# Kernel optimization log

Measured on AMD Instinct MI355X. Metric: run time of the kernel, lower is better.

Reference implementation:

```python
import jax, jax.numpy as jnp
import numpy as np

D_MODEL = 1024
NUM_HEADS = 16
MAX_LEN = 2048
D_HEAD = D_MODEL // NUM_HEADS
BATCH = 2
SEQ = 2048


def setup_inputs() -> dict:
    key = jax.random.key(0)
    ks = jax.random.split(key, 8)
    s = 1.0 / np.sqrt(D_MODEL)
    return {
        "x": jax.random.normal(ks[0], (BATCH, SEQ, D_MODEL), dtype=jnp.float32),
        "Wq": jax.random.uniform(ks[1], (D_MODEL, D_MODEL), jnp.float32, -s, s),
        "bq": jax.random.uniform(ks[2], (D_MODEL,), jnp.float32, -s, s),
        "Wk": jax.random.uniform(ks[3], (D_MODEL, D_MODEL), jnp.float32, -s, s),
        "bk": jax.random.uniform(ks[4], (D_MODEL,), jnp.float32, -s, s),
        "Wv": jax.random.uniform(ks[5], (D_MODEL, D_MODEL), jnp.float32, -s, s),
        "bv": jax.random.uniform(ks[6], (D_MODEL,), jnp.float32, -s, s),
        "Er": jax.random.normal(ks[7], (MAX_LEN, D_HEAD), dtype=jnp.float32),
    }


def _skew(QEr):
    # QEr: [B, H, S, S]  (music-transformer skew trick)
    B, H, S, _ = QEr.shape
    padded = jnp.pad(QEr, ((0, 0), (0, 0), (0, 0), (1, 0)))  # [B,H,S,S+1]
    reshaped = padded.reshape(B, H, S + 1, S)
    return reshaped[:, :, 1:, :]  # [B,H,S,S]


def reference(x, Wq, bq, Wk, bk, Wv, bv, Er):
    B, S, D = x.shape
    H, Dh = NUM_HEADS, D_HEAD
    # projections (torch Linear: x @ W.T + b)
    q = (jnp.einsum('bsd,ed->bse', x, Wq) + bq).reshape(B, S, H, Dh).transpose(0, 2, 1, 3)
    k = (jnp.einsum('bsd,ed->bse', x, Wk) + bk).reshape(B, S, H, Dh).transpose(0, 2, 1, 3)
    v = (jnp.einsum('bsd,ed->bse', x, Wv) + bv).reshape(B, S, H, Dh).transpose(0, 2, 1, 3)
    # relative position scores
    Er_slice = Er[MAX_LEN - S:, :]                    # [S, Dh]
    QEr = jnp.einsum('bhsd,td->bhst', q, Er_slice)    # [B,H,S,S]
    Srel = _skew(QEr)
    QKt = jnp.einsum('bhsd,bhtd->bhst', q, k)
    attn = (QKt + Srel) / jnp.sqrt(jnp.asarray(Dh, x.dtype))
    causal = jnp.tril(jnp.ones((S, S), dtype=bool))
    attn = jnp.where(causal[None, None], attn, -jnp.inf)
    attn = jax.nn.softmax(attn, axis=-1)
    out = jnp.einsum('bhst,bhtd->bhsd', attn, v)      # [B,H,S,Dh]
    out = out.transpose(0, 2, 1, 3).reshape(B, S, D)
    return out  # dropout is identity in eval mode
```

## Files before the change

kernel.cpp:

```cpp
#include <hip/hip_runtime.h>
#include <hip/hip_bf16.h>

constexpr int B  = 2;
constexpr int S  = 2048;
constexpr int D  = 1024;
constexpr int H  = 16;

typedef unsigned short u16t;
typedef unsigned long long u64;
typedef __attribute__((ext_vector_type(8))) short short8;
typedef __attribute__((ext_vector_type(4))) float float4v;

__device__ __forceinline__ float b2f(u16t u) {
    union { unsigned int i; float f; } c; c.i = ((unsigned int)u) << 16; return c.f;
}
__device__ __forceinline__ u16t f2b(float f) {
    __hip_bfloat16 h = __float2bfloat16(f);
    union { __hip_bfloat16 h; u16t u; } c; c.h = h; return c.u;
}
__device__ __forceinline__ u64 pack4(float4 v) {
    return (u64)f2b(v.x) | ((u64)f2b(v.y) << 16) | ((u64)f2b(v.z) << 32) | ((u64)f2b(v.w) << 48);
}

constexpr size_t XB_OFF = 0;
constexpr size_t WQ_OFF = 4194304;
constexpr size_t WK_OFF = 5242880;
constexpr size_t WV_OFF = 6291456;
constexpr size_t ER_OFF = 7340032;
constexpr size_t QW_OFF = 7471104;
constexpr size_t KW_OFF = 11665408;
constexpr size_t VT_OFF = 15859712;

__global__ __launch_bounds__(256) void prep_bf16(
    const float* __restrict__ x,  const float* __restrict__ Wq,
    const float* __restrict__ Wk, const float* __restrict__ Wv,
    const float* __restrict__ Er, u64* __restrict__ dst)
{
    size_t i4 = (size_t)blockIdx.x * 256 + threadIdx.x;
    const float* src; size_t off;
    if      (i4 < 1048576) { src = x;  off = i4; }
    else if (i4 < 1310720) { src = Wq; off = i4 - 1048576; }
    else if (i4 < 1572864) { src = Wk; off = i4 - 1310720; }
    else if (i4 < 1835008) { src = Wv; off = i4 - 1572864; }
    else                   { src = Er; off = i4 - 1835008; }
    float4 v = ((const float4*)src)[off];
    dst[i4] = pack4(v);
}

__global__ __launch_bounds__(256, 3) void qkv_mfma(
    const u16t* __restrict__ xb,
    const u16t* __restrict__ wqb, const u16t* __restrict__ wkb, const u16t* __restrict__ wvb,
    const float* __restrict__ bq, const float* __restrict__ bk, const float* __restrict__ bv,
    u16t* __restrict__ qo, u16t* __restrict__ ko, u16t* __restrict__ vT)
{
    const int z = blockIdx.z;
    const u16t*  W    = (z == 0) ? wqb : (z == 1) ? wkb : wvb;
    const float* bias = (z == 0) ? bq  : (z == 1) ? bk  : bv;

    __shared__ __align__(16) u16t Xs[128][72];
    __shared__ __align__(16) u16t Ws[128][72];

    const int tid = threadIdx.x;
    const int w = tid >> 6, lane = tid & 63;
    const int quad = lane >> 4, l16 = lane & 15;
    const int m0 = blockIdx.x * 128, n0 = blockIdx.y * 128;
    const int mi = (w >> 1) * 64, ni = (w & 1) * 64;

    float4v acc[4][4];
    #pragma unroll
    for (int mt = 0; mt < 4; ++mt)
        #pragma unroll
        for (int nt = 0; nt < 4; ++nt) acc[mt][nt] = (float4v){0.f, 0.f, 0.f, 0.f};

    for (int k0 = 0; k0 < D; k0 += 64) {
        short8 xa[4], wa[4];
        #pragma unroll
        for (int it = 0; it < 4; ++it) {
            int idx = tid + it * 256, r = idx >> 3, c = idx & 7;
            xa[it] = *(const short8*)&xb[(size_t)(m0 + r) * D + k0 + c * 8];
            wa[it] = *(const short8*)&W [(size_t)(n0 + r) * D + k0 + c * 8];
        }
        __syncthreads();
        #pragma unroll
        for (int it = 0; it < 4; ++it) {
            int idx = tid + it * 256, r = idx >> 3, c = idx & 7;
            *(short8*)&Xs[r][c * 8] = xa[it];
            *(short8*)&Ws[r][c * 8] = wa[it];
        }
        __syncthreads();
        short8 af[4][2], bf[4][2];
        #pragma unroll
        for (int mt = 0; mt < 4; ++mt) {
            af[mt][0] = *(const short8*)&Xs[mi + mt * 16 + l16][quad * 8];
            af[mt][1] = *(const short8*)&Xs[mi + mt * 16 + l16][quad * 8 + 32];
        }
        #pragma unroll
        for (int nt = 0; nt < 4; ++nt) {
            bf[nt][0] = *(const short8*)&Ws[ni + nt * 16 + l16][quad * 8];
            bf[nt][1] = *(const short8*)&Ws[ni + nt * 16 + l16][quad * 8 + 32];
        }
        #pragma unroll
        for (int mt = 0; mt < 4; ++mt)
            #pragma unroll
            for (int nt = 0; nt < 4; ++nt) {
                acc[mt][nt] = __builtin_amdgcn_mfma_f32_16x16x32_bf16(af[mt][0], bf[nt][0], acc[mt][nt], 0, 0, 0);
                acc[mt][nt] = __builtin_amdgcn_mfma_f32_16x16x32_bf16(af[mt][1], bf[nt][1], acc[mt][nt], 0, 0, 0);
            }
    }

    float bias_v[4];
    #pragma unroll
    for (int nt = 0; nt < 4; ++nt) bias_v[nt] = bias[n0 + ni + nt * 16 + l16];

    #pragma unroll
    for (int mt = 0; mt < 4; ++mt)
        #pragma unroll
        for (int nt = 0; nt < 4; ++nt) {
            int n = n0 + ni + nt * 16 + l16;
            int h = n >> 6, dh = n & 63;
            int mb = m0 + mi + mt * 16 + quad * 4;
            int b_ = mb >> 11, s = mb & (S - 1);
            if (z == 2) {
                float4 o;
                o.x = acc[mt][nt][0] + bias_v[nt];
                o.y = acc[mt][nt][1] + bias_v[nt];
                o.z = acc[mt][nt][2] + bias_v[nt];
                o.w = acc[mt][nt][3] + bias_v[nt];
                *(u64*)&vT[((size_t)(b_ * H + h) * 64 + dh) * S + s] = pack4(o);
            } else {
                u16t* out = (z == 0) ? qo : ko;
                #pragma unroll
                for (int rg = 0; rg < 4; ++rg)
                    out[((size_t)(b_ * H + h) * S + s + rg) * 64 + dh] =
                        f2b(acc[mt][nt][rg] + bias_v[nt]);
            }
        }
}

__global__ __launch_bounds__(256, 4) void attn_mfma(
    const u16t* __restrict__ q, const u16t* __restrict__ k,
    const u16t* __restrict__ vT, const u16t* __restrict__ er,
    float* __restrict__ out)
{
    __shared__ __align__(16) u16t KsS[64 * 64];
    __shared__ __align__(16) u16t VsS[64 * 64];
    __shared__ __align__(16) u16t PsS[64 * 64];
    __shared__ float lrows[64];
    char* KsB = (char*)KsS;
    char* VsB = (char*)VsS;
    char* PsB = (char*)PsS;

    const int tid = threadIdx.x;
    const int w = tid >> 6, lane = tid & 63;
    const int quad = lane >> 4, l16 = lane & 15;
    const int bh = blockIdx.x;
    const int ix = (int)gridDim.y - 1 - (int)blockIdx.y;
    const int s0 = ix * 64;
    const int hh = bh & (H - 1), bb = bh >> 4;

    const u16t* qb = q  + (size_t)bh * S * 64;
    const u16t* kb = k  + (size_t)bh * S * 64;
    const u16t* vb = vT + (size_t)bh * 64 * S;

    const size_t qoff = (size_t)(s0 + w * 16 + l16) * 64;
    const short8 Qa0 = *(const short8*)&qb[qoff + quad * 8];
    const short8 Qa1 = *(const short8*)&qb[qoff + 32 + quad * 8];

    float4v accO[4], L[5];
    #pragma unroll
    for (int t = 0; t < 4; ++t) accO[t] = (float4v){0.f, 0.f, 0.f, 0.f};
    float lsum[4] = {0.f, 0.f, 0.f, 0.f};

    const int xk = (l16 & 7);

    const float SC = 0.18033688f;
    const float M2 = 17.3125f;

    for (int jt = 0; jt <= ix; ++jt) {
        const int t0 = jt * 64;
        const int jbase = S - 64 - s0 + t0;
        const bool diag = (jt == ix);

        short8 kreg[2], vreg[2];
        int kpos[2];
        #pragma unroll
        for (int it = 0; it < 2; ++it) {
            int idx = tid + it * 256;
            int r = idx >> 3, c = idx & 7;
            kreg[it] = *(const short8*)&kb[(size_t)(t0 + r) * 64 + c * 8];
            kpos[it] = r * 128 + ((c ^ (r & 7)) << 4);
            vreg[it] = *(const short8*)&vb[(size_t)r * S + t0 + c * 8];
        }
        short8 ef0[4], ef1[4];
        #pragma unroll
        for (int c = 1; c <= 4; ++c) {
            int grow = jbase + (3 - w + c) * 16 + l16;
            if (grow > S - 1) grow = S - 1;
            const u16t* ep = &er[(size_t)grow * 64 + quad * 8];
            ef0[c - 1] = *(const short8*)ep;
            ef1[c - 1] = *(const short8*)(ep + 32);
        }

        __syncthreads();

        #pragma unroll
        for (int it = 0; it < 2; ++it) {
            *(short8*)(KsB + kpos[it]) = kreg[it];
            *(short8*)(VsB + kpos[it]) = vreg[it];
        }
        __syncthreads();

        float4v S1[4];
        #pragma unroll
        for (int nt = 0; nt < 4; ++nt) {
            int row = nt * 16 + l16;
            short8 b0 = *(const short8*)(KsB + row * 128 + ((quad ^ xk) << 4));
            short8 b1 = *(const short8*)(KsB + row * 128 + (((quad + 4) ^ xk) << 4));
            float4v a = (float4v){0.f, 0.f, 0.f, 0.f};
            a = __builtin_amdgcn_mfma_f32_16x16x32_bf16(Qa0, b0, a, 0, 0, 0);
            a = __builtin_amdgcn_mfma_f32_16x16x32_bf16(Qa1, b1, a, 0, 0, 0);
            S1[nt] = a;
        }

        if (jt == 0) {
            int grow = jbase + (3 - w) * 16 + l16;
            if (grow > S - 1) grow = S - 1;
            const u16t* ep = &er[(size_t)grow * 64 + quad * 8];
            short8 e0 = *(const short8*)ep;
            short8 e1 = *(const short8*)(ep + 32);
            float4v e = (float4v){0.f, 0.f, 0.f, 0.f};
            e = __builtin_amdgcn_mfma_f32_16x16x32_bf16(Qa0, e0, e, 0, 0, 0);
            e = __builtin_amdgcn_mfma_f32_16x16x32_bf16(Qa1, e1, e, 0, 0, 0);
            L[0] = e;
        } else {
            L[0] = L[4];
        }
        #pragma unroll
        for (int c = 1; c <= 4; ++c) {
            float4v e = (float4v){0.f, 0.f, 0.f, 0.f};
            e = __builtin_amdgcn_mfma_f32_16x16x32_bf16(Qa0, ef0[c - 1], e, 0, 0, 0);
            e = __builtin_amdgcn_mfma_f32_16x16x32_bf16(Qa1, ef1[c - 1], e, 0, 0, 0);
            L[c] = e;
        }

        #pragma unroll
        for (int rg = 0; rg < 4; ++rg) {
            const int usel = quad * 4 + rg;
            const int thr = 15 - usel;
            const int sidx = ((lane & 48) | ((l16 + thr) & 15)) * 4;
            const bool give_lo = (l16 >= thr);
            const int i_ = w * 16 + usel;
            const int ikey = i_ & 7;
            float psum = 0.f;
            #pragma unroll
            for (int nt = 0; nt < 4; ++nt) {
                float prov = give_lo ? L[nt][rg] : L[nt + 1][rg];
                float qe = __int_as_float(
                    __builtin_amdgcn_ds_bpermute(sidx, __float_as_int(prov)));
                float s2 = fmaf(S1[nt][rg] + qe, SC, -M2);
                float p = (diag && (nt * 16 + l16 > i_ - w * 16 + w * 16) && (nt * 16 + l16 > w * 16 + usel))
                              ? 0.f : exp2f(s2);
                p = (diag && (nt * 16 + l16 > w * 16 + usel)) ? 0.f : p;
                psum += p;
                int j_ = nt * 16 + l16;
                *(u16t*)(PsB + i_ * 128 + (((j_ >> 3) ^ ikey) << 4) + (j_ & 7) * 2) = f2b(p);
            }
            lsum[rg] += psum;
        }

        {
            int ar = w * 16 + l16;
            short8 pa0 = *(const short8*)(PsB + ar * 128 + ((quad ^ (ar & 7)) << 4));
            short8 pa1 = *(const short8*)(PsB + ar * 128 + (((quad + 4) ^ (ar & 7)) << 4));
            #pragma unroll
            for (int td = 0; td < 4; ++td) {
                int row = td * 16 + l16;
                short8 a0 = *(const short8*)(VsB + row * 128 + ((quad ^ xk) << 4));
                short8 a1 = *(const short8*)(VsB + row * 128 + (((quad + 4) ^ xk) << 4));
                accO[td] = __builtin_amdgcn_mfma_f32_16x16x32_bf16(a0, pa0, accO[td], 0, 0, 0);
                accO[td] = __builtin_amdgcn_mfma_f32_16x16x32_bf16(a1, pa1, accO[td], 0, 0, 0);
            }
        }
    }

    #pragma unroll
    for (int rg = 0; rg < 4; ++rg) {
        float s = lsum[rg];
        s += __shfl_xor(s, 1);
        s += __shfl_xor(s, 2);
        s += __shfl_xor(s, 4);
        s += __shfl_xor(s, 8);
        if (l16 == 0) lrows[w * 16 + quad * 4 + rg] = s;
    }
    float inv = 1.f / lrows[w * 16 + l16];

    float* ob = out + (size_t)bb * S * D + (size_t)hh * 64
                + (size_t)(s0 + w * 16 + l16) * D;
    #pragma unroll
    for (int td = 0; td < 4; ++td) {
        float4 o;
        o.x = accO[td][0] * inv;
        o.y = accO[td][1] * inv;
        o.z = accO[td][2] * inv;
        o.w = accO[td][3] * inv;
        *(float4*)&ob[td * 16 + quad * 4] = o;
    }
}

extern "C" void kernel_launch(void* const* d_in, const int* in_sizes, int n_in,
                              void* d_out, int out_size, void* d_ws, size_t ws_size,
                              hipStream_t stream) {
    const float* x  = (const float*)d_in[0];
    const float* Wq = (const float*)d_in[1];
    const float* bq = (const float*)d_in[2];
    const float* Wk = (const float*)d_in[3];
    const float* bk = (const float*)d_in[4];
    const float* Wv = (const float*)d_in[5];
    const float* bv = (const float*)d_in[6];
    const float* Er = (const float*)d_in[7];
    float* out = (float*)d_out;

    u16t* ws16 = (u16t*)d_ws;
    u16t* xb  = ws16 + XB_OFF;
    u16t* wqb = ws16 + WQ_OFF;
    u16t* wkb = ws16 + WK_OFF;
    u16t* wvb = ws16 + WV_OFF;
    u16t* erb = ws16 + ER_OFF;
    u16t* qw  = ws16 + QW_OFF;
    u16t* kw  = ws16 + KW_OFF;
    u16t* vTw = ws16 + VT_OFF;

    prep_bf16<<<dim3(7296), dim3(256), 0, stream>>>(x, Wq, Wk, Wv, Er, (u64*)d_ws);

    qkv_mfma<<<dim3(32, 8, 3), dim3(256), 0, stream>>>(
        xb, wqb, wkb, wvb, bq, bk, bv, qw, kw, vTw);

    attn_mfma<<<dim3(32, 32), dim3(256), 0, stream>>>(qw, kw, vTw, erb, out);
}
```

Before: 211.6 us.

## Double-buffer K/V via global_load_lds, pair causal tiles per block, prefetch QKV GEMM

```diff
diff --git a/kernel.cpp b/kernel.cpp
--- a/kernel.cpp
+++ b/kernel.cpp
@@ -11,15 +11,24 @@
 typedef __attribute__((ext_vector_type(8))) short short8;
 typedef __attribute__((ext_vector_type(4))) float float4v;
 
-__device__ __forceinline__ float b2f(u16t u) {
-    union { unsigned int i; float f; } c; c.i = ((unsigned int)u) << 16; return c.f;
+__device__ __forceinline__ float b2f(unsigned int u) {
+    union { unsigned int i; float f; } c; c.i = u << 16; return c.f;
 }
 __device__ __forceinline__ u16t f2b(float f) {
     __hip_bfloat16 h = __float2bfloat16(f);
     union { __hip_bfloat16 h; u16t u; } c; c.h = h; return c.u;
 }
+__device__ __forceinline__ unsigned int pkbf(float a, float b) {
+    return (unsigned int)f2b(a) | ((unsigned int)f2b(b) << 16);
+}
 __device__ __forceinline__ u64 pack4(float4 v) {
     return (u64)f2b(v.x) | ((u64)f2b(v.y) << 16) | ((u64)f2b(v.z) << 32) | ((u64)f2b(v.w) << 48);
+}
+
+typedef __attribute__((address_space(1))) const unsigned int* as1_u32p;
+typedef __attribute__((address_space(3))) unsigned int* as3_u32p;
+__device__ __forceinline__ void gll16(const void* g, void* l) {
+    __builtin_amdgcn_global_load_lds((as1_u32p)g, (as3_u32p)l, 16, 0, 0);
 }
 
 constexpr size_t XB_OFF = 0;
@@ -72,14 +81,15 @@
         #pragma unroll
         for (int nt = 0; nt < 4; ++nt) acc[mt][nt] = (float4v){0.f, 0.f, 0.f, 0.f};
 
+    short8 xa[4], wa[4];
+    #pragma unroll
+    for (int it = 0; it < 4; ++it) {
+        int idx = tid + it * 256, r = idx >> 3, c = idx & 7;
+        xa[it] = *(const short8*)&xb[(size_t)(m0 + r) * D + c * 8];
+        wa[it] = *(const short8*)&W [(size_t)(n0 + r) * D + c * 8];
+    }
+
     for (int k0 = 0; k0 < D; k0 += 64) {
-        short8 xa[4], wa[4];
-        #pragma unroll
-        for (int it = 0; it < 4; ++it) {
-            int idx = tid + it * 256, r = idx >> 3, c = idx & 7;
-            xa[it] = *(const short8*)&xb[(size_t)(m0 + r) * D + k0 + c * 8];
-            wa[it] = *(const short8*)&W [(size_t)(n0 + r) * D + k0 + c * 8];
-        }
         __syncthreads();
         #pragma unroll
         for (int it = 0; it < 4; ++it) {
@@ -88,6 +98,14 @@
             *(short8*)&Ws[r][c * 8] = wa[it];
         }
         __syncthreads();
+        if (k0 + 64 < D) {
+            #pragma unroll
+            for (int it = 0; it < 4; ++it) {
+                int idx = tid + it * 256, r = idx >> 3, c = idx & 7;
+                xa[it] = *(const short8*)&xb[(size_t)(m0 + r) * D + k0 + 64 + c * 8];
+                wa[it] = *(const short8*)&W [(size_t)(n0 + r) * D + k0 + 64 + c * 8];
+            }
+        }
         short8 af[4][2], bf[4][2];
         #pragma unroll
         for (int mt = 0; mt < 4; ++mt) {
@@ -142,8 +160,8 @@
     const u16t* __restrict__ vT, const u16t* __restrict__ er,
     float* __restrict__ out)
 {
-    __shared__ __align__(16) u16t KsS[64 * 64];
-    __shared__ __align__(16) u16t VsS[64 * 64];
+    __shared__ __align__(16) u16t KsS[2][64 * 64];
+    __shared__ __align__(16) u16t VsS[2][64 * 64];
     __shared__ __align__(16) u16t PsS[64 * 64];
     __shared__ float lrows[64];
     char* KsB = (char*)KsS;
@@ -154,156 +172,169 @@
     const int w = tid >> 6, lane = tid & 63;
     const int quad = lane >> 4, l16 = lane & 15;
     const int bh = blockIdx.x;
-    const int ix = (int)gridDim.y - 1 - (int)blockIdx.y;
-    const int s0 = ix * 64;
+    const int pr = blockIdx.y;
     const int hh = bh & (H - 1), bb = bh >> 4;
 
     const u16t* qb = q  + (size_t)bh * S * 64;
     const u16t* kb = k  + (size_t)bh * S * 64;
     const u16t* vb = vT + (size_t)bh * 64 * S;
 
-    const size_t qoff = (size_t)(s0 + w * 16 + l16) * 64;
-    const short8 Qa0 = *(const short8*)&qb[qoff + quad * 8];
-    const short8 Qa1 = *(const short8*)&qb[qoff + 32 + quad * 8];
-
-    float4v accO[4], L[5];
-    #pragma unroll
-    for (int t = 0; t < 4; ++t) accO[t] = (float4v){0.f, 0.f, 0.f, 0.f};
-    float lsum[4] = {0.f, 0.f, 0.f, 0.f};
-
     const int xk = (l16 & 7);
-
     const float SC = 0.18033688f;
     const float M2 = 17.3125f;
 
-    for (int jt = 0; jt <= ix; ++jt) {
-        const int t0 = jt * 64;
-        const int jbase = S - 64 - s0 + t0;
-        const bool diag = (jt == ix);
-
-        short8 kreg[2], vreg[2];
-        int kpos[2];
+    const int srow = lane >> 3;
+    const int d8s  = (lane & 7) ^ (srow & 7);
+
+    #pragma unroll 1
+    for (int ph = 0; ph < 2; ++ph) {
+        const int ix = ph ? (31 - pr) : pr;
+        const int s0 = ix * 64;
+
+        const size_t qoff = (size_t)(s0 + w * 16 + l16) * 64;
+        const short8 Qa0 = *(const short8*)&qb[qoff + quad * 8];
+        const short8 Qa1 = *(const short8*)&qb[qoff + 32 + quad * 8];
+
+        float4v accO[4], L[5];
+        #pragma unroll
+        for (int t = 0; t < 4; ++t) accO[t] = (float4v){0.f, 0.f, 0.f, 0.f};
+        float lsum[4] = {0.f, 0.f, 0.f, 0.f};
+
         #pragma unroll
         for (int it = 0; it < 2; ++it) {
-            int idx = tid + it * 256;
-            int r = idx >> 3, c = idx & 7;
-            kreg[it] = *(const short8*)&kb[(size_t)(t0 + r) * 64 + c * 8];
-            kpos[it] = r * 128 + ((c ^ (r & 7)) << 4);
-            vreg[it] = *(const short8*)&vb[(size_t)r * S + t0 + c * 8];
-        }
-        short8 ef0[4], ef1[4];
-        #pragma unroll
-        for (int c = 1; c <= 4; ++c) {
-            int grow = jbase + (3 - w + c) * 16 + l16;
-            if (grow > S - 1) grow = S - 1;
-            const u16t* ep = &er[(size_t)grow * 64 + quad * 8];
-            ef0[c - 1] = *(const short8*)ep;
-            ef1[c - 1] = *(const short8*)(ep + 32);
-        }
-
+            int ci = w * 2 + it;
+            int prow = ci * 8 + srow;
+            gll16(&kb[(size_t)prow * 64 + d8s * 8], KsB + ci * 1024);
+            gll16(&vb[(size_t)prow * S + d8s * 8], VsB + ci * 1024);
+        }
         __syncthreads();
 
-        #pragma unroll
-        for (int it = 0; it < 2; ++it) {
-            *(short8*)(KsB + kpos[it]) = kreg[it];
-            *(short8*)(VsB + kpos[it]) = vreg[it];
-        }
-        __syncthreads();
-
-        float4v S1[4];
-        #pragma unroll
-        for (int nt = 0; nt < 4; ++nt) {
-            int row = nt * 16 + l16;
-            short8 b0 = *(const short8*)(KsB + row * 128 + ((quad ^ xk) << 4));
-            short8 b1 = *(const short8*)(KsB + row * 128 + (((quad + 4) ^ xk) << 4));
-            float4v a = (float4v){0.f, 0.f, 0.f, 0.f};
-            a = __builtin_amdgcn_mfma_f32_16x16x32_bf16(Qa0, b0, a, 0, 0, 0);
-            a = __builtin_amdgcn_mfma_f32_16x16x32_bf16(Qa1, b1, a, 0, 0, 0);
-            S1[nt] = a;
-        }
-
-        if (jt == 0) {
-            int grow = jbase + (3 - w) * 16 + l16;
-            if (grow > S - 1) grow = S - 1;
-            const u16t* ep = &er[(size_t)grow * 64 + quad * 8];
-            short8 e0 = *(const short8*)ep;
-            short8 e1 = *(const short8*)(ep + 32);
-            float4v e = (float4v){0.f, 0.f, 0.f, 0.f};
-            e = __builtin_amdgcn_mfma_f32_16x16x32_bf16(Qa0, e0, e, 0, 0, 0);
-            e = __builtin_amdgcn_mfma_f32_16x16x32_bf16(Qa1, e1, e, 0, 0, 0);
-            L[0] = e;
-        } else {
-            L[0] = L[4];
-        }
-        #pragma unroll
-        for (int c = 1; c <= 4; ++c) {
-            float4v e = (float4v){0.f, 0.f, 0.f, 0.f};
-            e = __builtin_amdgcn_mfma_f32_16x16x32_bf16(Qa0, ef0[c - 1], e, 0, 0, 0);
-            e = __builtin_amdgcn_mfma_f32_16x16x32_bf16(Qa1, ef1[c - 1], e, 0, 0, 0);
-            L[c] = e;
+        for (int jt = 0; jt <= ix; ++jt) {
+            const int t0 = jt * 64;
+            const int jbase = S - 64 - s0 + t0;
+            const bool diag = (jt == ix);
+            const int bsel = (jt & 1) * 8192;
+
+            short8 ef0[4], ef1[4], e00, e01;
+            #pragma unroll
+            for (int c = 1; c <= 4; ++c) {
+                int grow = jbase + (3 - w + c) * 16 + l16;
+                if (grow > S - 1) grow = S - 1;
+                const u16t* ep = &er[(size_t)grow * 64 + quad * 8];
+                ef0[c - 1] = *(const short8*)ep;
+                ef1[c - 1] = *(const short8*)(ep + 32);
+            }
+            if (jt == 0) {
+                int grow = jbase + (3 - w) * 16 + l16;
+                if (grow > S - 1) grow = S - 1;
+                const u16t* ep = &er[(size_t)grow * 64 + quad * 8];
+                e00 = *(const short8*)ep;
+                e01 = *(const short8*)(ep + 32);
+            }
+
+            if (jt < ix) {
+                int nb = ((jt + 1) & 1) * 8192;
+                #pragma unroll
+                for (int it = 0; it < 2; ++it) {
+                    int ci = w * 2 + it;
+                    int prow = ci * 8 + srow;
+                    gll16(&kb[(size_t)(t0 + 64 + prow) * 64 + d8s * 8], KsB + nb + ci * 1024);
+                    gll16(&vb[(size_t)prow * S + t0 + 64 + d8s * 8], VsB + nb + ci * 1024);
+                }
+            }
+
+            float4v S1[4];
+            #pragma unroll
+            for (int nt = 0; nt < 4; ++nt) {
+                int row = nt * 16 + l16;
+                short8 b0 = *(const short8*)(KsB + bsel + row * 128 + ((quad ^ xk) << 4));
+                short8 b1 = *(const short8*)(KsB + bsel + row * 128 + (((quad + 4) ^ xk) << 4));
+                float4v a = (float4v){0.f, 0.f, 0.f, 0.f};
+                a = __builtin_amdgcn_mfma_f32_16x16x32_bf16(Qa0, b0, a, 0, 0, 0);
+                a = __builtin_amdgcn_mfma_f32_16x16x32_bf16(Qa1, b1, a, 0, 0, 0);
+                S1[nt] = a;
+            }
+
+            if (jt == 0) {
+                float4v e = (float4v){0.f, 0.f, 0.f, 0.f};
+                e = __builtin_amdgcn_mfma_f32_16x16x32_bf16(Qa0, e00, e, 0, 0, 0);
+                e = __builtin_amdgcn_mfma_f32_16x16x32_bf16(Qa1, e01, e, 0, 0, 0);
+                L[0] = e;
+            } else {
+                L[0] = L[4];
+            }
+            #pragma unroll
+            for (int c = 1; c <= 4; ++c) {
+                float4v e = (float4v){0.f, 0.f, 0.f, 0.f};
+                e = __builtin_amdgcn_mfma_f32_16x16x32_bf16(Qa0, ef0[c - 1], e, 0, 0, 0);
+                e = __builtin_amdgcn_mfma_f32_16x16x32_bf16(Qa1, ef1[c - 1], e, 0, 0, 0);
+                L[c] = e;
+            }
+
+            #pragma unroll
+            for (int rg = 0; rg < 4; ++rg) {
+                const int usel = quad * 4 + rg;
+                const int thr = 15 - usel;
+                const int sidx = ((lane & 48) | ((l16 + thr) & 15)) * 4;
+                const bool give_lo = (l16 >= thr);
+                unsigned int p01 = give_lo ? pkbf(L[0][rg], L[1][rg]) : pkbf(L[1][rg], L[2][rg]);
+                unsigned int p23 = give_lo ? pkbf(L[2][rg], L[3][rg]) : pkbf(L[3][rg], L[4][rg]);
+                unsigned int q01 = (unsigned int)__builtin_amdgcn_ds_bpermute(sidx, (int)p01);
+                unsigned int q23 = (unsigned int)__builtin_amdgcn_ds_bpermute(sidx, (int)p23);
+                float qe[4] = { b2f(q01 & 0xffffu), b2f(q01 >> 16),
+                                b2f(q23 & 0xffffu), b2f(q23 >> 16) };
+                const int i_ = w * 16 + usel;
+                const int ikey = i_ & 7;
+                float psum = 0.f;
+                #pragma unroll
+                for (int nt = 0; nt < 4; ++nt) {
+                    float s2 = fmaf(S1[nt][rg] + qe[nt], SC, -M2);
+                    float p = (diag && (nt * 16 + l16 > i_)) ? 0.f : exp2f(s2);
+                    psum += p;
+                    int j_ = nt * 16 + l16;
+                    *(u16t*)(PsB + i_ * 128 + (((j_ >> 3) ^ ikey) << 4) + (j_ & 7) * 2) = f2b(p);
+                }
+                lsum[rg] += psum;
+            }
+
+            {
+                int ar = w * 16 + l16;
+                short8 pa0 = *(const short8*)(PsB + ar * 128 + ((quad ^ (ar & 7)) << 4));
+                short8 pa1 = *(const short8*)(PsB + ar * 128 + (((quad + 4) ^ (ar & 7)) << 4));
+                #pragma unroll
+                for (int td = 0; td < 4; ++td) {
+                    int row = td * 16 + l16;
+                    short8 a0 = *(const short8*)(VsB + bsel + row * 128 + ((quad ^ xk) << 4));
+                    short8 a1 = *(const short8*)(VsB + bsel + row * 128 + (((quad + 4) ^ xk) << 4));
+                    accO[td] = __builtin_amdgcn_mfma_f32_16x16x32_bf16(a0, pa0, accO[td], 0, 0, 0);
+                    accO[td] = __builtin_amdgcn_mfma_f32_16x16x32_bf16(a1, pa1, accO[td], 0, 0, 0);
+                }
+            }
+            __syncthreads();
         }
 
         #pragma unroll
         for (int rg = 0; rg < 4; ++rg) {
-            const int usel = quad * 4 + rg;
-            const int thr = 15 - usel;
-            const int sidx = ((lane & 48) | ((l16 + thr) & 15)) * 4;
-            const bool give_lo = (l16 >= thr);
-            const int i_ = w * 16 + usel;
-            const int ikey = i_ & 7;
-            float psum = 0.f;
-            #pragma unroll
-            for (int nt = 0; nt < 4; ++nt) {
-                float prov = give_lo ? L[nt][rg] : L[nt + 1][rg];
-                float qe = __int_as_float(
-                    __builtin_amdgcn_ds_bpermute(sidx, __float_as_int(prov)));
-                float s2 = fmaf(S1[nt][rg] + qe, SC, -M2);
-                float p = (diag && (nt * 16 + l16 > i_ - w * 16 + w * 16) && (nt * 16 + l16 > w * 16 + usel))
-                              ? 0.f : exp2f(s2);
-                p = (diag && (nt * 16 + l16 > w * 16 + usel)) ? 0.f : p;
-                psum += p;
-                int j_ = nt * 16 + l16;
-                *(u16t*)(PsB + i_ * 128 + (((j_ >> 3) ^ ikey) << 4) + (j_ & 7) * 2) = f2b(p);
-            }
-            lsum[rg] += psum;
-        }
-
-        {
-            int ar = w * 16 + l16;
-            short8 pa0 = *(const short8*)(PsB + ar * 128 + ((quad ^ (ar & 7)) << 4));
-            short8 pa1 = *(const short8*)(PsB + ar * 128 + (((quad + 4) ^ (ar & 7)) << 4));
-            #pragma unroll
-            for (int td = 0; td < 4; ++td) {
-                int row = td * 16 + l16;
-                short8 a0 = *(const short8*)(VsB + row * 128 + ((quad ^ xk) << 4));
-                short8 a1 = *(const short8*)(VsB + row * 128 + (((quad + 4) ^ xk) << 4));
-                accO[td] = __builtin_amdgcn_mfma_f32_16x16x32_bf16(a0, pa0, accO[td], 0, 0, 0);
-                accO[td] = __builtin_amdgcn_mfma_f32_16x16x32_bf16(a1, pa1, accO[td], 0, 0, 0);
-            }
-        }
-    }
-
-    #pragma unroll
-    for (int rg = 0; rg < 4; ++rg) {
-        float s = lsum[rg];
-        s += __shfl_xor(s, 1);
-        s += __shfl_xor(s, 2);
-        s += __shfl_xor(s, 4);
-        s += __shfl_xor(s, 8);
-        if (l16 == 0) lrows[w * 16 + quad * 4 + rg] = s;
-    }
-    float inv = 1.f / lrows[w * 16 + l16];
-
-    float* ob = out + (size_t)bb * S * D + (size_t)hh * 64
-                + (size_t)(s0 + w * 16 + l16) * D;
-    #pragma unroll
-    for (int td = 0; td < 4; ++td) {
-        float4 o;
-        o.x = accO[td][0] * inv;
-        o.y = accO[td][1] * inv;
-        o.z = accO[td][2] * inv;
-        o.w = accO[td][3] * inv;
-        *(float4*)&ob[td * 16 + quad * 4] = o;
+            float s = lsum[rg];
+            s += __shfl_xor(s, 1);
+            s += __shfl_xor(s, 2);
+            s += __shfl_xor(s, 4);
+            s += __shfl_xor(s, 8);
+            if (l16 == 0) lrows[w * 16 + quad * 4 + rg] = s;
+        }
+        float inv = 1.f / lrows[w * 16 + l16];
+
+        float* ob = out + (size_t)bb * S * D + (size_t)hh * 64
+                    + (size_t)(s0 + w * 16 + l16) * D;
+        #pragma unroll
+        for (int td = 0; td < 4; ++td) {
+            float4 o;
+            o.x = accO[td][0] * inv;
+            o.y = accO[td][1] * inv;
+            o.z = accO[td][2] * inv;
+            o.w = accO[td][3] * inv;
+            *(float4*)&ob[td * 16 + quad * 4] = o;
+        }
     }
 }
 
@@ -335,5 +366,5 @@
     qkv_mfma<<<dim3(32, 8, 3), dim3(256), 0, stream>>>(
         xb, wqb, wkb, wvb, bq, bk, bv, qw, kw, vTw);
 
-    attn_mfma<<<dim3(32, 32), dim3(256), 0, stream>>>(qw, kw, vTw, erb, out);
-}
+    attn_mfma<<<dim3(32, 16), dim3(256), 0, stream>>>(qw, kw, vTw, erb, out);
+}
```

After: 202.8 us. 1.04x faster.
